# Performance work log

Hardware: AMD Instinct MI355X
Metric: run time of the kernel (lower is better)

## Reference

```python
import jax, jax.numpy as jnp
import numpy as np

B_COMMITMENT = 1.0


def setup_inputs() -> dict:
    key = jax.random.key(0)
    k1, k2 = jax.random.split(key)
    inpt = jax.random.normal(k1, (16, 1024, 256), dtype=jnp.float32)
    emb_mtrx = jax.random.normal(k2, (256, 8192), dtype=jnp.float32) * 0.05
    return {"inpt": inpt, "emb_mtrx": emb_mtrx}


def reference(inpt, emb_mtrx):
    D = inpt.shape[-1]
    x = inpt.reshape(-1, D)  # [N, D]
    # squared L2 distance to every code: [N, K]
    dist = (
        jnp.sum(x * x, axis=1, keepdims=True)
        - 2.0 * (x @ emb_mtrx)
        + jnp.sum(emb_mtrx * emb_mtrx, axis=0, keepdims=True)
    )
    idx = jnp.argmin(dist, axis=1).reshape(inpt.shape[:-1])  # [B, T]
    q = jnp.take(emb_mtrx.T, idx, axis=0)  # [B, T, D] gather of nearest codes
    l_commitment = jnp.mean((jax.lax.stop_gradient(q) - inpt) ** 2)
    l_codebook = jnp.mean((q - jax.lax.stop_gradient(inpt)) ** 2)
    loss = B_COMMITMENT * l_commitment + l_codebook
    q_st = inpt + jax.lax.stop_gradient(q - inpt)  # straight-through
    return q_st, loss
```

## Files before the change

### kernel.cpp

```cpp
#include <hip/hip_runtime.h>
#include <hip/hip_bf16.h>
#include <cstdint>


typedef __bf16 bf16x8 __attribute__((ext_vector_type(8)));
typedef __bf16 bf16x4 __attribute__((ext_vector_type(4)));
typedef float  f32x16 __attribute__((ext_vector_type(16)));

#define N_ROWS  16384
#define N_CODES 8192
#define DDIM    256
#define NT      16
#define BUFB    32768

#define STAGE16(gptr, lptr) __builtin_amdgcn_global_load_lds( \
    (const __attribute__((address_space(1))) void*)(gptr),    \
    (__attribute__((address_space(3))) void*)(lptr), 16, 0, 0)

#define SBAR() do { asm volatile("" ::: "memory"); \
                    __builtin_amdgcn_s_barrier();  \
                    asm volatile("" ::: "memory"); } while (0)
#define WAITVM(N) asm volatile("s_waitcnt vmcnt(" #N ")" ::: "memory")

__global__ void prep_x_k(const float* __restrict__ x,
                         __bf16* __restrict__ xhi, __bf16* __restrict__ xlo) {
  int i = blockIdx.x * 256 + threadIdx.x;
  float4 v = reinterpret_cast<const float4*>(x)[i];
  float a[4] = {v.x, v.y, v.z, v.w};
  bf16x4 h, l;
#pragma unroll
  for (int j = 0; j < 4; ++j) {
    __bf16 hh = (__bf16)a[j];
    h[j] = hh;
    l[j] = (__bf16)(a[j] - (float)hh);
  }
  reinterpret_cast<bf16x4*>(xhi)[i] = h;
  reinterpret_cast<bf16x4*>(xlo)[i] = l;
}

__global__ void prep_e_k(const float* __restrict__ emb,
                         __bf16* __restrict__ ehi, __bf16* __restrict__ elo,
                         float* __restrict__ embT) {
  __shared__ float tile[64][65];
  const int kb = blockIdx.x * 64, db = blockIdx.y * 64;
  const int t = threadIdx.x;
  const int tk = t & 63, td = t >> 6;
#pragma unroll
  for (int c = 0; c < 16; ++c) {
    int d = c * 4 + td;
    tile[d][tk] = emb[(size_t)(db + d) * N_CODES + kb + tk];
  }
  __syncthreads();
#pragma unroll
  for (int c = 0; c < 16; ++c) {
    int k = c * 4 + td;
    int d = tk;
    float v = tile[d][k];
    size_t o = (size_t)(kb + k) * DDIM + db + d;
    __bf16 h = (__bf16)v;
    embT[o] = v;
    ehi[o] = h;
    elo[o] = (__bf16)(v - (float)h);
  }
}

__global__ void enorm_k(const float* __restrict__ emb, float* __restrict__ enorm) {
  int k = blockIdx.x * 256 + threadIdx.x;
  float s = 0.f;
  for (int d = 0; d < DDIM; ++d) {
    float v = emb[(size_t)d * N_CODES + k];
    s += v * v;
  }
  enorm[k] = s;
}

__global__ __launch_bounds__(512, 2) void vq_main_k(
    const __bf16* __restrict__ xhi, const __bf16* __restrict__ xlo,
    const __bf16* __restrict__ ehi, const __bf16* __restrict__ elo,
    const float* __restrict__ enorm, unsigned long long* __restrict__ keys) {
  extern __shared__ __align__(16) unsigned char smem[];

  const int tid = threadIdx.x;
  const int wid = tid >> 6, lane = tid & 63;
  const int cg = wid >> 2, rg = wid & 3;
  const int l31 = lane & 31, lh = lane >> 5;

  const int orig = blockIdx.x;
  const int j = orig >> 3;
  const int bm = (orig & 7) * 8 + (j & 7);
  const int bn = j >> 3;

  const int cbase = bn * 256 + cg * 128 + lh * 4;
  f32x16 acc[4][2];
#pragma unroll
  for (int c = 0; c < 4; ++c) {
    f32x16 ci;
#pragma unroll
    for (int q = 0; q < 4; ++q)
#pragma unroll
      for (int r = 0; r < 4; ++r)
        ci[q * 4 + r] = -0.5f * enorm[cbase + c * 32 + q * 8 + r];
    acc[c][0] = ci; acc[c][1] = ci;
  }
  __builtin_amdgcn_sched_barrier(0);

  const size_t aoff = (size_t)(bm * 256 + wid * 32 + l31) * 512 + (size_t)lh * 16;
  const size_t boff = (size_t)(bn * 256 + wid * 32 + l31) * 512 + (size_t)lh * 16;
  const char* pxh = (const char*)xhi + aoff;
  const char* pxl = (const char*)xlo + aoff;
  const char* peh = (const char*)ehi + boff;
  const char* pel = (const char*)elo + boff;
  const int dxh = wid * 1024, dxl = 8192 + wid * 1024;
  const int deh = 16384 + wid * 1024, del = 24576 + wid * 1024;

  const int xrd = rg * 2048 + lane * 16;
  const int erd = 16384 + cg * 4096 + lane * 16;

#pragma unroll
  for (int s = 0; s < 3; ++s) {
    unsigned char* bs = smem + s * BUFB;
    STAGE16(pxh + s * 32, bs + dxh);
    STAGE16(pxl + s * 32, bs + dxl);
    STAGE16(peh + s * 32, bs + deh);
    STAGE16(pel + s * 32, bs + del);
  }
  WAITVM(8);
  SBAR();

#pragma unroll 1
  for (int t = 0; t < NT; ++t) {
    int s = t + 3; if (s >= NT) s -= NT;
    const unsigned char* rb = smem + (t & 3) * BUFB;
    unsigned char* wb = smem + (s & 3) * BUFB;
    const size_t kb = (size_t)s * 32;

    STAGE16(pxh + kb, wb + dxh);
    STAGE16(pxl + kb, wb + dxl);
    STAGE16(peh + kb, wb + deh);
    STAGE16(pel + kb, wb + del);

    bf16x8 ehf[4], xhf[2], xlf[2], elf[4];
#pragma unroll
    for (int c = 0; c < 4; ++c) ehf[c] = *(const bf16x8*)(rb + erd + c * 1024);
#pragma unroll
    for (int r = 0; r < 2; ++r) xhf[r] = *(const bf16x8*)(rb + xrd + r * 1024);
#pragma unroll
    for (int r = 0; r < 2; ++r) xlf[r] = *(const bf16x8*)(rb + 8192 + xrd + r * 1024);
#pragma unroll
    for (int c = 0; c < 4; ++c) elf[c] = *(const bf16x8*)(rb + 8192 + erd + c * 1024);

#pragma unroll
    for (int c = 0; c < 4; ++c)
#pragma unroll
      for (int r = 0; r < 2; ++r)
        acc[c][r] = __builtin_amdgcn_mfma_f32_32x32x16_bf16(ehf[c], xhf[r], acc[c][r], 0, 0, 0);
#pragma unroll
    for (int c = 0; c < 4; ++c)
#pragma unroll
      for (int r = 0; r < 2; ++r)
        acc[c][r] = __builtin_amdgcn_mfma_f32_32x32x16_bf16(ehf[c], xlf[r], acc[c][r], 0, 0, 0);
#pragma unroll
    for (int c = 0; c < 4; ++c)
#pragma unroll
      for (int r = 0; r < 2; ++r)
        acc[c][r] = __builtin_amdgcn_mfma_f32_32x32x16_bf16(elf[c], xhf[r], acc[c][r], 0, 0, 0);

    WAITVM(8);
    SBAR();
  }
  WAITVM(0);

#pragma unroll
  for (int r = 0; r < 2; ++r) {
    float bv = -3.4e38f;
    unsigned bcode = 0;
#pragma unroll
    for (int c = 0; c < 4; ++c)
#pragma unroll
      for (int q = 0; q < 4; ++q)
#pragma unroll
        for (int rr = 0; rr < 4; ++rr) {
          float v = acc[c][r][q * 4 + rr];
          unsigned cd = (unsigned)(cbase + c * 32 + q * 8 + rr);
          if (v > bv) { bv = v; bcode = cd; }
        }
    unsigned u = __float_as_uint(bv);
    u = (u & 0x80000000u) ? ~u : (u | 0x80000000u);
    unsigned long long key =
        ((unsigned long long)u << 32) | (unsigned)(0xFFFFFFFFu ^ bcode);
    unsigned olo = __shfl_xor((unsigned)key, 32, 64);
    unsigned ohi = __shfl_xor((unsigned)(key >> 32), 32, 64);
    unsigned long long okey = ((unsigned long long)ohi << 32) | olo;
    if (okey > key) key = okey;
    if (lane < 32)
      atomicMax(&keys[bm * 256 + rg * 64 + r * 32 + l31], key);
  }
}

__global__ void gather_k(const float* __restrict__ x, const float* __restrict__ embT,
                         const unsigned long long* __restrict__ keys,
                         float* __restrict__ qout, float* __restrict__ rowsum) {
  const int row = blockIdx.x;
  const int lane = threadIdx.x;
  const unsigned low = (unsigned)(keys[row] & 0xffffffffull);
  const int idx = (int)(~low);
  float4 q  = reinterpret_cast<const float4*>(embT + (size_t)idx * DDIM)[lane];
  float4 xv = reinterpret_cast<const float4*>(x + (size_t)row * DDIM)[lane];
  reinterpret_cast<float4*>(qout + (size_t)row * DDIM)[lane] = q;
  float dx = q.x - xv.x, dy = q.y - xv.y, dz = q.z - xv.z, dw = q.w - xv.w;
  float s = dx * dx + dy * dy + dz * dz + dw * dw;
#pragma unroll
  for (int mk = 32; mk; mk >>= 1) s += __shfl_xor(s, mk, 64);
  if (lane == 0) rowsum[row] = s;
}

__global__ void loss_k(const float* __restrict__ rowsum, float* __restrict__ out) {
  __shared__ float sm[4];
  const int t = threadIdx.x;
  float s = 0.f;
  for (int j = t; j < N_ROWS; j += 256) s += rowsum[j];
#pragma unroll
  for (int mk = 32; mk; mk >>= 1) s += __shfl_xor(s, mk, 64);
  if ((t & 63) == 0) sm[t >> 6] = s;
  __syncthreads();
  if (t == 0) out[0] = 2.0f * (sm[0] + sm[1] + sm[2] + sm[3]) / (float)(N_ROWS * DDIM);
}

extern "C" void kernel_launch(void* const* d_in, const int* in_sizes, int n_in,
                              void* d_out, int out_size, void* d_ws, size_t ws_size,
                              hipStream_t stream) {
  const float* x   = (const float*)d_in[0];
  const float* emb = (const float*)d_in[1];
  float* qout = (float*)d_out;

  char* w = (char*)d_ws;
  unsigned long long* keys = (unsigned long long*)w;
  float* rowsum = (float*)(w + 131072);
  __bf16* xhi = (__bf16*)(w + 196608);
  __bf16* xlo = xhi + (size_t)N_ROWS * DDIM;
  __bf16* ehi = xlo + (size_t)N_ROWS * DDIM;
  __bf16* elo = ehi + (size_t)N_CODES * DDIM;
  float*  embT = (float*)(elo + (size_t)N_CODES * DDIM);
  float*  enorm = embT + (size_t)N_CODES * DDIM;

  hipFuncSetAttribute((const void*)vq_main_k,
                      hipFuncAttributeMaxDynamicSharedMemorySize, 4 * BUFB);

  hipMemsetAsync(keys, 0, N_ROWS * sizeof(unsigned long long), stream);
  prep_x_k<<<4096, 256, 0, stream>>>(x, xhi, xlo);
  prep_e_k<<<dim3(N_CODES / 64, DDIM / 64), 256, 0, stream>>>(emb, ehi, elo, embT);
  enorm_k<<<N_CODES / 256, 256, 0, stream>>>(emb, enorm);
  vq_main_k<<<2048, 512, 4 * BUFB, stream>>>(xhi, xlo, ehi, elo, enorm, keys);
  gather_k<<<N_ROWS, 64, 0, stream>>>(x, embT, keys, qout, rowsum);
  loss_k<<<1, 256, 0, stream>>>(rowsum, qout + (size_t)N_ROWS * DDIM);
}
```

Measured before the change: 254.2 us.

## Drop LDS staging and load MFMA operands directly from global memory

Removes the four-stage LDS ring buffer (global_load_lds staging, vmcnt waits and block barriers) from the distance GEMM. Each wave now loads its bf16 hi/lo fragments straight from global memory into registers inside a fully unrolled K loop. Blocks shrink from 512 to 256 threads with a 256-row by 128-code tile, so the grid doubles. This removes barrier and LDS traffic, but operand sharing between waves now depends on the L1/L2 caches, and global load latency is only hidden by compiler scheduling and occupancy.

```diff
diff --git a/kernel.cpp b/kernel.cpp
--- a/kernel.cpp
+++ b/kernel.cpp
@@ -11,16 +11,6 @@
 #define N_CODES 8192
 #define DDIM    256
 #define NT      16
-#define BUFB    32768
-
-#define STAGE16(gptr, lptr) __builtin_amdgcn_global_load_lds( \
-    (const __attribute__((address_space(1))) void*)(gptr),    \
-    (__attribute__((address_space(3))) void*)(lptr), 16, 0, 0)
-
-#define SBAR() do { asm volatile("" ::: "memory"); \
-                    __builtin_amdgcn_s_barrier();  \
-                    asm volatile("" ::: "memory"); } while (0)
-#define WAITVM(N) asm volatile("s_waitcnt vmcnt(" #N ")" ::: "memory")
 
 __global__ void prep_x_k(const float* __restrict__ x,
                          __bf16* __restrict__ xhi, __bf16* __restrict__ xlo) {
@@ -74,23 +64,21 @@
   enorm[k] = s;
 }
 
-__global__ __launch_bounds__(512, 2) void vq_main_k(
+__global__ __launch_bounds__(256, 2) void vq_main_k(
     const __bf16* __restrict__ xhi, const __bf16* __restrict__ xlo,
     const __bf16* __restrict__ ehi, const __bf16* __restrict__ elo,
     const float* __restrict__ enorm, unsigned long long* __restrict__ keys) {
-  extern __shared__ __align__(16) unsigned char smem[];
-
   const int tid = threadIdx.x;
   const int wid = tid >> 6, lane = tid & 63;
-  const int cg = wid >> 2, rg = wid & 3;
+  const int rg = wid;
   const int l31 = lane & 31, lh = lane >> 5;
 
   const int orig = blockIdx.x;
   const int j = orig >> 3;
-  const int bm = (orig & 7) * 8 + (j & 7);
-  const int bn = j >> 3;
-
-  const int cbase = bn * 256 + cg * 128 + lh * 4;
+  const int grp = (orig & 7) * 8 + (j & 7);
+  const int p = j >> 3;
+
+  const int cbase = p * 128 + lh * 4;
   f32x16 acc[4][2];
 #pragma unroll
   for (int c = 0; c < 4; ++c) {
@@ -102,53 +90,25 @@
         ci[q * 4 + r] = -0.5f * enorm[cbase + c * 32 + q * 8 + r];
     acc[c][0] = ci; acc[c][1] = ci;
   }
-  __builtin_amdgcn_sched_barrier(0);
-
-  const size_t aoff = (size_t)(bm * 256 + wid * 32 + l31) * 512 + (size_t)lh * 16;
-  const size_t boff = (size_t)(bn * 256 + wid * 32 + l31) * 512 + (size_t)lh * 16;
-  const char* pxh = (const char*)xhi + aoff;
-  const char* pxl = (const char*)xlo + aoff;
-  const char* peh = (const char*)ehi + boff;
-  const char* pel = (const char*)elo + boff;
-  const int dxh = wid * 1024, dxl = 8192 + wid * 1024;
-  const int deh = 16384 + wid * 1024, del = 24576 + wid * 1024;
-
-  const int xrd = rg * 2048 + lane * 16;
-  const int erd = 16384 + cg * 4096 + lane * 16;
-
-#pragma unroll
-  for (int s = 0; s < 3; ++s) {
-    unsigned char* bs = smem + s * BUFB;
-    STAGE16(pxh + s * 32, bs + dxh);
-    STAGE16(pxl + s * 32, bs + dxl);
-    STAGE16(peh + s * 32, bs + deh);
-    STAGE16(pel + s * 32, bs + del);
-  }
-  WAITVM(8);
-  SBAR();
-
-#pragma unroll 1
+
+  const size_t eoff = (size_t)(p * 128 + l31) * DDIM + lh * 8;
+  const size_t xoff = (size_t)(grp * 256 + rg * 64 + l31) * DDIM + lh * 8;
+
+#pragma unroll
   for (int t = 0; t < NT; ++t) {
-    int s = t + 3; if (s >= NT) s -= NT;
-    const unsigned char* rb = smem + (t & 3) * BUFB;
-    unsigned char* wb = smem + (s & 3) * BUFB;
-    const size_t kb = (size_t)s * 32;
-
-    STAGE16(pxh + kb, wb + dxh);
-    STAGE16(pxl + kb, wb + dxl);
-    STAGE16(peh + kb, wb + deh);
-    STAGE16(pel + kb, wb + del);
-
-    bf16x8 ehf[4], xhf[2], xlf[2], elf[4];
-#pragma unroll
-    for (int c = 0; c < 4; ++c) ehf[c] = *(const bf16x8*)(rb + erd + c * 1024);
-#pragma unroll
-    for (int r = 0; r < 2; ++r) xhf[r] = *(const bf16x8*)(rb + xrd + r * 1024);
-#pragma unroll
-    for (int r = 0; r < 2; ++r) xlf[r] = *(const bf16x8*)(rb + 8192 + xrd + r * 1024);
-#pragma unroll
-    for (int c = 0; c < 4; ++c) elf[c] = *(const bf16x8*)(rb + 8192 + erd + c * 1024);
-
+    const size_t ke = eoff + t * 16;
+    const size_t kx = xoff + t * 16;
+    bf16x8 ehf[4], elf[4], xhf[2], xlf[2];
+#pragma unroll
+    for (int c = 0; c < 4; ++c) {
+      ehf[c] = *(const bf16x8*)(ehi + ke + c * 8192);
+      elf[c] = *(const bf16x8*)(elo + ke + c * 8192);
+    }
+#pragma unroll
+    for (int r = 0; r < 2; ++r) {
+      xhf[r] = *(const bf16x8*)(xhi + kx + r * 8192);
+      xlf[r] = *(const bf16x8*)(xlo + kx + r * 8192);
+    }
 #pragma unroll
     for (int c = 0; c < 4; ++c)
 #pragma unroll
@@ -164,11 +124,7 @@
 #pragma unroll
       for (int r = 0; r < 2; ++r)
         acc[c][r] = __builtin_amdgcn_mfma_f32_32x32x16_bf16(elf[c], xhf[r], acc[c][r], 0, 0, 0);
-
-    WAITVM(8);
-    SBAR();
-  }
-  WAITVM(0);
+  }
 
 #pragma unroll
   for (int r = 0; r < 2; ++r) {
@@ -193,7 +149,7 @@
     unsigned long long okey = ((unsigned long long)ohi << 32) | olo;
     if (okey > key) key = okey;
     if (lane < 32)
-      atomicMax(&keys[bm * 256 + rg * 64 + r * 32 + l31], key);
+      atomicMax(&keys[grp * 256 + rg * 64 + r * 32 + l31], key);
   }
 }
 
@@ -243,14 +199,11 @@
   float*  embT = (float*)(elo + (size_t)N_CODES * DDIM);
   float*  enorm = embT + (size_t)N_CODES * DDIM;
 
-  hipFuncSetAttribute((const void*)vq_main_k,
-                      hipFuncAttributeMaxDynamicSharedMemorySize, 4 * BUFB);
-
   hipMemsetAsync(keys, 0, N_ROWS * sizeof(unsigned long long), stream);
   prep_x_k<<<4096, 256, 0, stream>>>(x, xhi, xlo);
   prep_e_k<<<dim3(N_CODES / 64, DDIM / 64), 256, 0, stream>>>(emb, ehi, elo, embT);
   enorm_k<<<N_CODES / 256, 256, 0, stream>>>(emb, enorm);
-  vq_main_k<<<2048, 512, 4 * BUFB, stream>>>(xhi, xlo, ehi, elo, enorm, keys);
+  vq_main_k<<<4096, 256, 0, stream>>>(xhi, xlo, ehi, elo, enorm, keys);
   gather_k<<<N_ROWS, 64, 0, stream>>>(x, embT, keys, qout, rowsum);
   loss_k<<<1, 256, 0, stream>>>(rowsum, qout + (size_t)N_ROWS * DDIM);
 }
```

Result: slower. 406.5 us (+59.9%).
